# Kernel tuning notes

Hardware: AMD Instinct MI355X
Metric: run time of the kernel (lower is better)

## Reference

```python
import jax, jax.numpy as jnp
import numpy as np

N, E, G = 50000, 500000, 64
F_IN, H, C = 10, 4, 64
HC = H * C  # 256
NCLS = 8
BN_EPS = 1e-5


def _bn(x, g, b, m, v):
    # eval-mode BatchNorm1d with running stats
    return (x - m) * jax.lax.rsqrt(v + BN_EPS) * g + b


def _gat(x, src, dst, W, a_s, a_d, b):
    # PyG GATConv (concat=True): h=[N,H,C]; e_ij=leakyrelu(a_s.h_j + a_d.h_i);
    # softmax over incoming edges of each destination node; scatter-add.
    n = x.shape[0]
    h = (x @ W).reshape(n, H, C)
    es = jnp.einsum('nhc,hc->nh', h, a_s)  # source term per node
    ed = jnp.einsum('nhc,hc->nh', h, a_d)  # dest term per node
    e = jax.nn.leaky_relu(es[src] + ed[dst], 0.2)            # [E2,H]
    m = jax.ops.segment_max(e, dst, num_segments=n)
    ex = jnp.exp(e - m[dst])
    s = jax.ops.segment_sum(ex, dst, num_segments=n)
    alpha = ex / (s[dst] + 1e-16)                             # [E2,H]
    out = jax.ops.segment_sum(h[src] * alpha[:, :, None], dst, num_segments=n)
    return out.reshape(n, HC) + b, alpha


def _gcn(x, src, dst, W, b):
    n = x.shape[0]
    deg = jax.ops.segment_sum(jnp.ones_like(src, dtype=x.dtype), dst, num_segments=n)
    dinv = jax.lax.rsqrt(jnp.maximum(deg, 1.0))
    norm = dinv[src] * dinv[dst]
    xw = x @ W
    return jax.ops.segment_sum(xw[src] * norm[:, None], dst, num_segments=n) + b


def setup_inputs() -> dict:
    key = jax.random.key(0)
    ks = jax.random.split(key, 48)
    r = lambda i, sh, sc=0.1: jax.random.normal(ks[i], sh, dtype=jnp.float32) * sc
    p = {}
    p['x'] = jax.random.normal(ks[0], (N, F_IN), dtype=jnp.float32)
    p['edge_index'] = jax.random.randint(ks[1], (2, E), 0, N, dtype=jnp.int32)
    p['batch'] = jnp.sort(jax.random.randint(ks[2], (N,), 0, G, dtype=jnp.int32))
    # GAT1
    p['W1'] = r(3, (F_IN, HC)); p['as1'] = r(4, (H, C)); p['ad1'] = r(5, (H, C)); p['bi1'] = r(6, (HC,))
    # GAT2
    p['W2'] = r(7, (HC, HC)); p['as2'] = r(8, (H, C)); p['ad2'] = r(9, (H, C)); p['bi2'] = r(10, (HC,))
    # BN running stats / affine
    for i, (nm, d) in enumerate([('bn1', HC), ('bn2', HC), ('bn3', C)]):
        k0 = 11 + 4 * i
        p[nm + '_g'] = 1.0 + r(k0, (d,))
        p[nm + '_b'] = r(k0 + 1, (d,))
        p[nm + '_m'] = r(k0 + 2, (d,))
        p[nm + '_v'] = 1.0 + jax.random.uniform(ks[k0 + 3], (d,), dtype=jnp.float32) * 0.5
    # GCN
    p['Wg'] = r(23, (HC, C)); p['bg'] = r(24, (C,))
    # reduce_dim
    p['Wr'] = r(25, (2 * C, C)); p['br'] = r(26, (C,))
    # rul head
    p['Wh1'] = r(27, (C, 32)); p['bh1'] = r(28, (32,))
    p['Wh2'] = r(29, (32, 16)); p['bh2'] = r(30, (16,))
    p['Wh3'] = r(31, (16, 1)); p['bh3'] = r(32, (1,))
    # location head
    p['Wl1'] = r(33, (C, 32)); p['bl1'] = r(34, (32,))
    p['Wl2'] = r(35, (32, NCLS)); p['bl2'] = r(36, (NCLS,))
    # energy head
    p['We1'] = r(37, (C, 16)); p['be1'] = r(38, (16,))
    p['We2'] = r(39, (16, 1)); p['be2'] = r(40, (1,))
    return p


def reference(x, edge_index, batch,
              W1, as1, ad1, bi1, W2, as2, ad2, bi2,
              bn1_g, bn1_b, bn1_m, bn1_v, bn2_g, bn2_b, bn2_m, bn2_v,
              bn3_g, bn3_b, bn3_m, bn3_v,
              Wg, bg, Wr, br,
              Wh1, bh1, Wh2, bh2, Wh3, bh3,
              Wl1, bl1, Wl2, bl2, We1, be1, We2, be2):
    n = x.shape[0]
    loop = jnp.arange(n, dtype=edge_index.dtype)
    src = jnp.concatenate([edge_index[0], loop])
    dst = jnp.concatenate([edge_index[1], loop])

    h, alpha1 = _gat(x, src, dst, W1, as1, ad1, bi1)
    h = jax.nn.elu(_bn(h, bn1_g, bn1_b, bn1_m, bn1_v))  # dropout = identity (eval)
    h, alpha2 = _gat(h, src, dst, W2, as2, ad2, bi2)
    h = jax.nn.elu(_bn(h, bn2_g, bn2_b, bn2_m, bn2_v))
    h = _gcn(h, src, dst, Wg, bg)
    h = jax.nn.elu(_bn(h, bn3_g, bn3_b, bn3_m, bn3_v))  # node embeddings [N,64]

    cnt = jax.ops.segment_sum(jnp.ones((n,), h.dtype), batch, num_segments=G)
    x_mean = jax.ops.segment_sum(h, batch, num_segments=G) / jnp.maximum(cnt, 1.0)[:, None]
    x_max = jax.ops.segment_max(h, batch, num_segments=G)
    x_max = jnp.where(cnt[:, None] > 0, x_max, 0.0)
    xg = jnp.concatenate([x_mean, x_max], axis=1) @ Wr + br  # [G,64]

    t = jax.nn.relu(xg @ Wh1 + bh1)
    t = jax.nn.relu(t @ Wh2 + bh2)
    rul = jax.nn.sigmoid(t @ Wh3 + bh3) * 100.0
    loc = jax.nn.relu(xg @ Wl1 + bl1) @ Wl2 + bl2
    en = jax.nn.relu(xg @ We1 + be1) @ We2 + be2
    return rul, loc, en, h, xg
```

## Files before the change

kernel.cpp:

```cpp
#include <hip/hip_runtime.h>
#include <math.h>

#define SCAN_BLK 1024
#define BN_EPS 1e-5f

typedef __attribute__((ext_vector_type(8))) short short8;
typedef __attribute__((ext_vector_type(4))) short short4v;
typedef __attribute__((ext_vector_type(4))) float f32x4;

__device__ __forceinline__ float eluf(float x){ return x > 0.f ? x : (expf(x) - 1.f); }
__device__ __forceinline__ unsigned short f2bf(float f){
  unsigned u = __float_as_uint(f);
  u += 0x7FFFu + ((u >> 16) & 1u);
  return (unsigned short)(u >> 16);
}
__device__ __forceinline__ float bf2f(unsigned short s){
  return __uint_as_float(((unsigned)s) << 16);
}
__device__ __forceinline__ unsigned fmap(float f){
  unsigned b = __float_as_uint(f);
  return (b & 0x80000000u) ? ~b : (b | 0x80000000u);
}
__device__ __forceinline__ float funmap(unsigned u){
  unsigned b = (u & 0x80000000u) ? (u ^ 0x80000000u) : ~u;
  return __uint_as_float(b);
}
__device__ __forceinline__ float lrelu(float a){ return a > 0.f ? a : 0.2f * a; }

__global__ void k_count(const int* __restrict__ ei, int* __restrict__ deg, int ne, int e2)
{
  int t = blockIdx.x * 256 + threadIdx.x;
  if (t >= e2) return;
  int dst = (t < ne) ? ei[ne + t] : t - ne;
  atomicAdd(&deg[dst], 1);
}

__global__ void k_scan1(const int* __restrict__ deg, int* __restrict__ rowptr,
                        int* __restrict__ partials, float* __restrict__ dinv, int n)
{
  __shared__ int sh[SCAN_BLK];
  int t = threadIdx.x, base = blockIdx.x * SCAN_BLK;
  int v = (base + t < n) ? deg[base + t] : 0;
  sh[t] = v;
  __syncthreads();
  for (int off = 1; off < SCAN_BLK; off <<= 1) {
    int u = 0;
    if (t >= off) u = sh[t - off];
    __syncthreads();
    if (t >= off) sh[t] += u;
    __syncthreads();
  }
  if (base + t < n) {
    rowptr[base + t] = sh[t] - v;
    dinv[base + t] = rsqrtf(fmaxf((float)v, 1.f));
  }
  if (t == SCAN_BLK - 1) partials[blockIdx.x] = sh[t];
}

__global__ void k_scan2(int* __restrict__ rowptr, const int* __restrict__ partials, int n)
{
  int base = blockIdx.x * SCAN_BLK;
  int add = 0;
  for (int i = 0; i < blockIdx.x; i++) add += partials[i];
  int t = threadIdx.x;
  if (base + t < n) rowptr[base + t] += add;
}

__global__ void k_fill(const int* __restrict__ ei, const int* __restrict__ rowptr,
                       int* __restrict__ cursor, int* __restrict__ col, int ne, int e2)
{
  int t = blockIdx.x * 256 + threadIdx.x;
  if (t >= e2) return;
  int src, dst;
  if (t < ne) { src = ei[t]; dst = ei[ne + t]; } else { src = dst = t - ne; }
  int pos = rowptr[dst] + atomicAdd(&cursor[dst], 1);
  col[pos] = src;
}

__global__ void k_pack(const float* __restrict__ W, unsigned short* __restrict__ Wp,
                       int N, int nct)
{
  int tid = threadIdx.x;
  int l = tid >> 3, j = tid & 7;
  int ct = blockIdx.x >> 3, ks = blockIdx.x & 7;
  int k = ks * 32 + (l >> 4) * 8 + j;
  int c = ct * 16 + (l & 15);
  Wp[(size_t)(ks * nct + ct) * 512 + tid] = f2bf(W[(size_t)k * N + c]);
}

__global__ void k_prep_all(const float* __restrict__ W1, const float* __restrict__ as1,
                           const float* __restrict__ ad1,
                           const float* __restrict__ W2, const float* __restrict__ as2,
                           const float* __restrict__ ad2,
                           const float* __restrict__ bi1, const float* __restrict__ g1,
                           const float* __restrict__ b1, const float* __restrict__ m1,
                           const float* __restrict__ v1,
                           const float* __restrict__ bi2, const float* __restrict__ g2,
                           const float* __restrict__ b2, const float* __restrict__ m2,
                           const float* __restrict__ v2,
                           float* __restrict__ Ws1, float* __restrict__ Wd1,
                           float* __restrict__ WasT,
                           float* __restrict__ A1, float* __restrict__ B1,
                           float* __restrict__ A2, float* __restrict__ B2)
{
  int t = threadIdx.x;
  if (blockIdx.x < 8) {
    int g = blockIdx.x * 256 + t;
    int half = g >= 1024, r = g & 1023;
    int i = r >> 2, h = r & 3;
    const float* a = half ? ad2 : as2;
    float s = 0.f;
    for (int c = 0; c < 64; c++) s += W2[(size_t)i * 256 + h * 64 + c] * a[h * 64 + c];
    WasT[(size_t)(half * 4 + h) * 256 + i] = s;
  } else {
    if (t < 80) {
      int half = t / 40, r = t % 40;
      int k = r / 4, h = r % 4;
      const float* a = half ? ad1 : as1;
      float s = 0.f;
      for (int c = 0; c < 64; c++) s += W1[k * 256 + h * 64 + c] * a[h * 64 + c];
      (half ? Wd1 : Ws1)[k * 4 + h] = s;
    }
    if (t < 256) {
      float a = rsqrtf(v1[t] + BN_EPS) * g1[t];
      A1[t] = a; B1[t] = (bi1[t] - m1[t]) * a + b1[t];
      a = rsqrtf(v2[t] + BN_EPS) * g2[t];
      A2[t] = a; B2[t] = (bi2[t] - m2[t]) * a + b2[t];
    }
  }
}

__global__ void k_es1(const float* __restrict__ x, const float* __restrict__ Ws1,
                      const float* __restrict__ Wd1,
                      float* __restrict__ es, float* __restrict__ ed, int n)
{
  int t = blockIdx.x * 256 + threadIdx.x;
  if (t >= n) return;
  float xr[10];
  #pragma unroll
  for (int k = 0; k < 10; k++) xr[k] = x[(size_t)t * 10 + k];
  float e0[4] = {0,0,0,0}, e1[4] = {0,0,0,0};
  #pragma unroll
  for (int k = 0; k < 10; k++) {
    #pragma unroll
    for (int h = 0; h < 4; h++) {
      e0[h] += xr[k] * Ws1[k * 4 + h];
      e1[h] += xr[k] * Wd1[k * 4 + h];
    }
  }
  *(float4*)&es[t * 4] = make_float4(e0[0], e0[1], e0[2], e0[3]);
  *(float4*)&ed[t * 4] = make_float4(e1[0], e1[1], e1[2], e1[3]);
}

__global__ void k_xagg(const int* __restrict__ rowptr, const int* __restrict__ deg,
                       const int* __restrict__ col,
                       const float* __restrict__ es, const float* __restrict__ ed,
                       const float* __restrict__ x, float* __restrict__ xa, int n)
{
  int d = blockIdx.x * 4 + (threadIdx.x >> 6);
  if (d >= n) return;
  int lane = threadIdx.x & 63;
  int slot = lane >> 4, k = lane & 15;
  int start = rowptr[d], cnt = deg[d];
  bool active = (k < 10);
  float4 edv = *(const float4*)&ed[d * 4];

  float a0 = 0.f, a1 = 0.f, a2 = 0.f, a3 = 0.f;
  float s0 = 0.f, s1 = 0.f, s2 = 0.f, s3 = 0.f;
  int i = slot;
  for (; i + 4 < cnt; i += 8) {
    int e0 = start + i, e1 = start + i + 4;
    int sa = col[e0], sb = col[e1];
    float4 u0 = *(const float4*)&es[sa * 4];
    float4 u1 = *(const float4*)&es[sb * 4];
    float x0 = active ? x[(size_t)sa * 10 + k] : 0.f;
    float x1 = active ? x[(size_t)sb * 10 + k] : 0.f;
    float ex;
    ex = expf(lrelu(u0.x + edv.x)); a0 += ex * x0; s0 += ex;
    ex = expf(lrelu(u0.y + edv.y)); a1 += ex * x0; s1 += ex;
    ex = expf(lrelu(u0.z + edv.z)); a2 += ex * x0; s2 += ex;
    ex = expf(lrelu(u0.w + edv.w)); a3 += ex * x0; s3 += ex;
    ex = expf(lrelu(u1.x + edv.x)); a0 += ex * x1; s0 += ex;
    ex = expf(lrelu(u1.y + edv.y)); a1 += ex * x1; s1 += ex;
    ex = expf(lrelu(u1.z + edv.z)); a2 += ex * x1; s2 += ex;
    ex = expf(lrelu(u1.w + edv.w)); a3 += ex * x1; s3 += ex;
  }
  if (i < cnt) {
    int e0 = start + i;
    int sa = col[e0];
    float4 u0 = *(const float4*)&es[sa * 4];
    float x0 = active ? x[(size_t)sa * 10 + k] : 0.f;
    float ex;
    ex = expf(lrelu(u0.x + edv.x)); a0 += ex * x0; s0 += ex;
    ex = expf(lrelu(u0.y + edv.y)); a1 += ex * x0; s1 += ex;
    ex = expf(lrelu(u0.z + edv.z)); a2 += ex * x0; s2 += ex;
    ex = expf(lrelu(u0.w + edv.w)); a3 += ex * x0; s3 += ex;
  }
  a0 += __shfl_xor(a0, 16, 64); a0 += __shfl_xor(a0, 32, 64);
  a1 += __shfl_xor(a1, 16, 64); a1 += __shfl_xor(a1, 32, 64);
  a2 += __shfl_xor(a2, 16, 64); a2 += __shfl_xor(a2, 32, 64);
  a3 += __shfl_xor(a3, 16, 64); a3 += __shfl_xor(a3, 32, 64);
  s0 += __shfl_xor(s0, 16, 64); s0 += __shfl_xor(s0, 32, 64);
  s1 += __shfl_xor(s1, 16, 64); s1 += __shfl_xor(s1, 32, 64);
  s2 += __shfl_xor(s2, 16, 64); s2 += __shfl_xor(s2, 32, 64);
  s3 += __shfl_xor(s3, 16, 64); s3 += __shfl_xor(s3, 32, 64);

  if (slot == 0 && active) {
    float* xo = &xa[(size_t)d * 40];
    xo[k]      = a0 / (s0 + 1e-16f);
    xo[10 + k] = a1 / (s1 + 1e-16f);
    xo[20 + k] = a2 / (s2 + 1e-16f);
    xo[30 + k] = a3 / (s3 + 1e-16f);
  }
}

__global__ void k_gemm_xa(const float* __restrict__ xa, const float* __restrict__ W1,
                          const float* __restrict__ A1, const float* __restrict__ B1,
                          const float* __restrict__ WasT,
                          unsigned short* __restrict__ actA,
                          float* __restrict__ es, float* __restrict__ ed, int n)
{
  __shared__ float xal[160];
  __shared__ float actl[4][256];
  int tid = threadIdx.x;
  int n0 = blockIdx.x * 4;
  if (tid < 160 && (size_t)n0 * 40 + tid < (size_t)n * 40)
    xal[tid] = xa[(size_t)n0 * 40 + tid];
  __syncthreads();
  int c = tid, h = c >> 6;
  float w[10];
  #pragma unroll
  for (int k = 0; k < 10; k++) w[k] = W1[k * 256 + c];
  float a1 = A1[c], b1 = B1[c];
  #pragma unroll
  for (int m = 0; m < 4; m++) {
    int nn = n0 + m;
    if (nn >= n) break;
    float acc = 0.f;
    #pragma unroll
    for (int k = 0; k < 10; k++) acc += xal[m * 40 + h * 10 + k] * w[k];
    float v = eluf(acc * a1 + b1);
    actl[m][c] = v;
    actA[(size_t)nn * 256 + c] = f2bf(v);
  }
  __syncthreads();
  int wave = tid >> 6, lane = tid & 63;
  int nn = n0 + wave;
  if (nn < n) {
    float e[8] = {0,0,0,0,0,0,0,0};
    int c0 = lane * 4;
    #pragma unroll
    for (int j = 0; j < 4; j++) {
      float av = actl[wave][c0 + j];
      #pragma unroll
      for (int q = 0; q < 8; q++) e[q] += av * WasT[q * 256 + c0 + j];
    }
    #pragma unroll
    for (int off = 1; off < 64; off <<= 1) {
      #pragma unroll
      for (int q = 0; q < 8; q++) e[q] += __shfl_xor(e[q], off, 64);
    }
    if (lane == 0) {
      *(float4*)&es[nn * 4] = make_float4(e[0], e[1], e[2], e[3]);
      *(float4*)&ed[nn * 4] = make_float4(e[4], e[5], e[6], e[7]);
    }
  }
}

__global__ void k_gat_gather(const int* __restrict__ rowptr, const int* __restrict__ deg,
                             const int* __restrict__ col,
                             const float* __restrict__ es, const float* __restrict__ ed,
                             const unsigned short* __restrict__ act,
                             unsigned short* __restrict__ outb, int n)
{
  int d = blockIdx.x * 4 + (threadIdx.x >> 6);
  if (d >= n) return;
  int lane = threadIdx.x & 63;
  int half = lane >> 5, l32 = lane & 31;
  int c8 = l32 * 8, head = l32 >> 3;
  int start = rowptr[d], cnt = deg[d];
  float edh = ed[d * 4 + head];

  float acc[8] = {0.f,0.f,0.f,0.f,0.f,0.f,0.f,0.f};
  float sex = 0.f;
  int T = (cnt > half) ? ((cnt - half + 1) >> 1) : 0;
  int ebase = start + half;
  int t = 0;
  for (; t + 4 <= T; t += 4) {
    int e0 = ebase + 2 * t, e1 = e0 + 2, e2 = e0 + 4, e3 = e0 + 6;
    int s0 = col[e0], s1 = col[e1], s2 = col[e2], s3 = col[e3];
    float x0 = expf(lrelu(es[s0 * 4 + head] + edh));
    float x1 = expf(lrelu(es[s1 * 4 + head] + edh));
    float x2 = expf(lrelu(es[s2 * 4 + head] + edh));
    float x3 = expf(lrelu(es[s3 * 4 + head] + edh));
    short8 h0 = *(const short8*)&act[(size_t)s0 * 256 + c8];
    short8 h1 = *(const short8*)&act[(size_t)s1 * 256 + c8];
    short8 h2 = *(const short8*)&act[(size_t)s2 * 256 + c8];
    short8 h3 = *(const short8*)&act[(size_t)s3 * 256 + c8];
    #pragma unroll
    for (int j = 0; j < 8; j++) {
      acc[j] += bf2f((unsigned short)h0[j]) * x0 + bf2f((unsigned short)h1[j]) * x1
              + bf2f((unsigned short)h2[j]) * x2 + bf2f((unsigned short)h3[j]) * x3;
    }
    sex += x0 + x1 + x2 + x3;
  }
  for (; t < T; t++) {
    int e0 = ebase + 2 * t;
    int s0 = col[e0];
    float x0 = expf(lrelu(es[s0 * 4 + head] + edh));
    short8 h0 = *(const short8*)&act[(size_t)s0 * 256 + c8];
    #pragma unroll
    for (int j = 0; j < 8; j++) acc[j] += bf2f((unsigned short)h0[j]) * x0;
    sex += x0;
  }
  #pragma unroll
  for (int j = 0; j < 8; j++)
    acc[j] += __shfl_xor(acc[j], 32, 64);
  sex += __shfl_xor(sex, 32, 64);

  if (half == 0) {
    float sv = 1.f / (sex + 1e-16f);
    short8 o;
    #pragma unroll
    for (int j = 0; j < 8; j++) o[j] = (short)f2bf(acc[j] * sv);
    *(short8*)&outb[(size_t)d * 256 + c8] = o;
  }
}

__global__ __launch_bounds__(256) void k_mfma_gemm2(
    const unsigned short* __restrict__ agg2, const unsigned short* __restrict__ Wp2,
    const unsigned short* __restrict__ Wpg,
    const float* __restrict__ Abn, const float* __restrict__ Bbn,
    unsigned short* __restrict__ xwb, int n)
{
  __shared__ unsigned short bsh[16 * 512];
  __shared__ unsigned short act2[64 * 264];
  int tid = threadIdx.x, wave = tid >> 6, lane = tid & 63;
  int l15 = lane & 15, lg = lane >> 4;
  int rbase = blockIdx.x * 64 + wave * 16;
  int arow = rbase + l15; if (arow > n - 1) arow = n - 1;
  const unsigned short* ap = &agg2[(size_t)arow * 256 + lg * 8];

  f32x4 acc[16];
  f32x4 z = {0.f, 0.f, 0.f, 0.f};
  #pragma unroll
  for (int ct = 0; ct < 16; ct++) acc[ct] = z;

  for (int ks = 0; ks < 8; ks++) {
    const unsigned short* src = Wp2 + (size_t)ks * 16 * 512 + wave * 16 * 128;
    short8 stg[4];
    #pragma unroll
    for (int c = 0; c < 4; c++)
      stg[c] = *(const short8*)(src + c * 512 + lane * 8);
    short8 a = *(const short8*)(ap + ks * 32);
    __syncthreads();
    #pragma unroll
    for (int c = 0; c < 4; c++)
      *(short8*)&bsh[wave * 16 * 128 + c * 512 + lane * 8] = stg[c];
    __syncthreads();
    #pragma unroll
    for (int ct = 0; ct < 16; ct++) {
      short8 b = *(const short8*)&bsh[(ct * 64 + lane) * 8];
      acc[ct] = __builtin_amdgcn_mfma_f32_16x16x32_bf16(a, b, acc[ct], 0, 0, 0);
    }
  }

  float abn[16], bbn[16];
  #pragma unroll
  for (int ct = 0; ct < 16; ct++) {
    abn[ct] = Abn[ct * 16 + l15];
    bbn[ct] = Bbn[ct * 16 + l15];
  }
  #pragma unroll
  for (int r = 0; r < 4; r++) {
    int row = rbase + lg * 4 + r;
    if (row < n) {
      int rl = wave * 16 + lg * 4 + r;
      #pragma unroll
      for (int ct = 0; ct < 16; ct++) {
        float v = eluf(acc[r < 0 ? 0 : ct][r] * abn[ct] + bbn[ct]);
        act2[rl * 264 + ct * 16 + l15] = f2bf(v);
      }
    }
  }
  __syncthreads();

  f32x4 acc2[4];
  #pragma unroll
  for (int ct = 0; ct < 4; ct++) acc2[ct] = z;
  const unsigned short* a2p = &act2[(wave * 16 + l15) * 264];
  #pragma unroll
  for (int ks = 0; ks < 8; ks++) {
    short8 a2 = *(const short8*)(a2p + ks * 32 + lg * 8);
    #pragma unroll
    for (int ct = 0; ct < 4; ct++) {
      short8 b = *(const short8*)&Wpg[(size_t)(ks * 4 + ct) * 512 + lane * 8];
      acc2[ct] = __builtin_amdgcn_mfma_f32_16x16x32_bf16(a2, b, acc2[ct], 0, 0, 0);
    }
  }
  #pragma unroll
  for (int r = 0; r < 4; r++) {
    int row = rbase + lg * 4 + r;
    if (row < n) {
      #pragma unroll
      for (int ct = 0; ct < 4; ct++)
        xwb[(size_t)row * 64 + ct * 16 + l15] = f2bf(acc2[ct][r]);
    }
  }
}

__global__ void k_gcn_gather(const int* __restrict__ rowptr, const int* __restrict__ deg,
                             const int* __restrict__ col, const float* __restrict__ dinv,
                             const unsigned short* __restrict__ xwb,
                             const float* __restrict__ bias,
                             const float* __restrict__ gg, const float* __restrict__ bb,
                             const float* __restrict__ mm, const float* __restrict__ vv,
                             float* __restrict__ hout, int n)
{
  int d = blockIdx.x * 4 + (threadIdx.x >> 6);
  if (d >= n) return;
  int lane = threadIdx.x & 63;
  int slot = lane >> 3, cg = (lane & 7) * 8;
  int start = rowptr[d], cnt = deg[d];
  float dinvd = rsqrtf(fmaxf((float)cnt, 1.f));

  float acc[8] = {0.f,0.f,0.f,0.f,0.f,0.f,0.f,0.f};
  int i = slot;
  for (; i + 8 < cnt; i += 16) {
    int s0 = col[start + i], s1 = col[start + i + 8];
    float n0 = dinv[s0], n1 = dinv[s1];
    short8 h0 = *(const short8*)&xwb[(size_t)s0 * 64 + cg];
    short8 h1 = *(const short8*)&xwb[(size_t)s1 * 64 + cg];
    #pragma unroll
    for (int j = 0; j < 8; j++)
      acc[j] += bf2f((unsigned short)h0[j]) * n0 + bf2f((unsigned short)h1[j]) * n1;
  }
  if (i < cnt) {
    int s0 = col[start + i];
    float n0 = dinv[s0];
    short8 h0 = *(const short8*)&xwb[(size_t)s0 * 64 + cg];
    #pragma unroll
    for (int j = 0; j < 8; j++)
      acc[j] += bf2f((unsigned short)h0[j]) * n0;
  }
  #pragma unroll
  for (int j = 0; j < 8; j++) {
    acc[j] += __shfl_xor(acc[j], 8, 64);
    acc[j] += __shfl_xor(acc[j], 16, 64);
    acc[j] += __shfl_xor(acc[j], 32, 64);
    acc[j] *= dinvd;
  }

  if (lane < 8) {
    float out[8];
    #pragma unroll
    for (int j = 0; j < 8; j++) {
      int c = cg + j;
      float r = ((acc[j] + bias[c]) - mm[c]) * rsqrtf(vv[c] + BN_EPS) * gg[c] + bb[c];
      out[j] = eluf(r);
    }
    *(float4*)&hout[(size_t)d * 64 + cg]     = make_float4(out[0], out[1], out[2], out[3]);
    *(float4*)&hout[(size_t)d * 64 + cg + 4] = make_float4(out[4], out[5], out[6], out[7]);
  }
}

__global__ void k_pool_partial(const float* __restrict__ hout, const int* __restrict__ batch,
                               float* __restrict__ psum, unsigned* __restrict__ pmaxu,
                               int n)
{
  int wave = threadIdx.x >> 6, lane = threadIdx.x & 63;
  int wbase = blockIdx.x * 128 + wave * 32;
  int wend = wbase + 32; if (wend > n) wend = n;
  if (wbase >= n) return;

  int g_cur = -1;
  float s = 0.f, mx = -1e30f;
  for (int node = wbase; node < wend; node++) {
    int g = batch[node];
    if (g != g_cur) {
      if (g_cur >= 0) {
        atomicAdd(&psum[g_cur * 64 + lane], s);
        atomicMax(&pmaxu[g_cur * 64 + lane], fmap(mx));
      }
      g_cur = g; s = 0.f; mx = -1e30f;
    }
    float v = hout[(size_t)node * 64 + lane];
    s += v;
    mx = fmaxf(mx, v);
  }
  if (g_cur >= 0) {
    atomicAdd(&psum[g_cur * 64 + lane], s);
    atomicMax(&pmaxu[g_cur * 64 + lane], fmap(mx));
  }
}

__global__ void k_heads(const float* __restrict__ psum, const unsigned* __restrict__ pmaxu,
                        const int* __restrict__ batch,
                        const float* __restrict__ Wr, const float* __restrict__ br,
                        const float* __restrict__ Wh1, const float* __restrict__ bh1,
                        const float* __restrict__ Wh2, const float* __restrict__ bh2,
                        const float* __restrict__ Wh3, const float* __restrict__ bh3,
                        const float* __restrict__ Wl1, const float* __restrict__ bl1,
                        const float* __restrict__ Wl2, const float* __restrict__ bl2,
                        const float* __restrict__ We1, const float* __restrict__ be1,
                        const float* __restrict__ We2, const float* __restrict__ be2,
                        float* __restrict__ outp, int n, int xg_off)
{
  __shared__ float cat[128], xg[64], t1[32], t2[16], l1[32], e1[16];
  int g = blockIdx.x, c = threadIdx.x;

  int lo = 0, hi = n;
  while (lo < hi) { int mid = (lo + hi) >> 1; if (batch[mid] < g) lo = mid + 1; else hi = mid; }
  int start = lo;
  lo = start; hi = n;
  while (lo < hi) { int mid = (lo + hi) >> 1; if (batch[mid] < g + 1) lo = mid + 1; else hi = mid; }
  int cntg = lo - start;

  float mean = psum[g * 64 + c] / fmaxf((float)cntg, 1.f);
  float mxv = (cntg > 0) ? funmap(pmaxu[g * 64 + c]) : 0.f;
  cat[c] = mean; cat[64 + c] = mxv;
  __syncthreads();
  float a = br[c];
  for (int i = 0; i < 128; i++) a += cat[i] * Wr[i * 64 + c];
  xg[c] = a;
  outp[xg_off + g * 64 + c] = a;
  __syncthreads();
  if (c < 32) {
    float u = bh1[c]; for (int i = 0; i < 64; i++) u += xg[i] * Wh1[i * 32 + c];
    t1[c] = fmaxf(u, 0.f);
    float v = bl1[c]; for (int i = 0; i < 64; i++) v += xg[i] * Wl1[i * 32 + c];
    l1[c] = fmaxf(v, 0.f);
  }
  __syncthreads();
  if (c < 16) {
    float u = bh2[c]; for (int i = 0; i < 32; i++) u += t1[i] * Wh2[i * 16 + c];
    t2[c] = fmaxf(u, 0.f);
    float v = be1[c]; for (int i = 0; i < 64; i++) v += xg[i] * We1[i * 16 + c];
    e1[c] = fmaxf(v, 0.f);
  }
  __syncthreads();
  if (c < 8) {
    float v = bl2[c]; for (int i = 0; i < 32; i++) v += l1[i] * Wl2[i * 8 + c];
    outp[64 + g * 8 + c] = v;
  }
  if (c == 0) {
    float u = bh3[0]; for (int i = 0; i < 16; i++) u += t2[i] * Wh3[i];
    outp[g] = 100.f / (1.f + expf(-u));
    float v = be2[0]; for (int i = 0; i < 16; i++) v += e1[i] * We2[i];
    outp[576 + g] = v;
  }
}

extern "C" void kernel_launch(void* const* d_in, const int* in_sizes, int n_in,
                              void* d_out, int out_size, void* d_ws, size_t ws_size,
                              hipStream_t stream)
{
  const float* x    = (const float*)d_in[0];
  const int*   ei   = (const int*)d_in[1];
  const int*   batch= (const int*)d_in[2];
  const float* W1   = (const float*)d_in[3];
  const float* as1  = (const float*)d_in[4];
  const float* ad1  = (const float*)d_in[5];
  const float* bi1  = (const float*)d_in[6];
  const float* W2   = (const float*)d_in[7];
  const float* as2  = (const float*)d_in[8];
  const float* ad2  = (const float*)d_in[9];
  const float* bi2  = (const float*)d_in[10];
  const float* bn1g = (const float*)d_in[11];
  const float* bn1b = (const float*)d_in[12];
  const float* bn1m = (const float*)d_in[13];
  const float* bn1v = (const float*)d_in[14];
  const float* bn2g = (const float*)d_in[15];
  const float* bn2b = (const float*)d_in[16];
  const float* bn2m = (const float*)d_in[17];
  const float* bn2v = (const float*)d_in[18];
  const float* bn3g = (const float*)d_in[19];
  const float* bn3b = (const float*)d_in[20];
  const float* bn3m = (const float*)d_in[21];
  const float* bn3v = (const float*)d_in[22];
  const float* Wg   = (const float*)d_in[23];
  const float* bg   = (const float*)d_in[24];
  const float* Wr   = (const float*)d_in[25];
  const float* br   = (const float*)d_in[26];
  const float* Wh1  = (const float*)d_in[27];
  const float* bh1  = (const float*)d_in[28];
  const float* Wh2  = (const float*)d_in[29];
  const float* bh2  = (const float*)d_in[30];
  const float* Wh3  = (const float*)d_in[31];
  const float* bh3  = (const float*)d_in[32];
  const float* Wl1  = (const float*)d_in[33];
  const float* bl1  = (const float*)d_in[34];
  const float* Wl2  = (const float*)d_in[35];
  const float* bl2  = (const float*)d_in[36];
  const float* We1  = (const float*)d_in[37];
  const float* be1  = (const float*)d_in[38];
  const float* We2  = (const float*)d_in[39];
  const float* be2  = (const float*)d_in[40];

  const int n  = in_sizes[2];
  const int ne = in_sizes[1] / 2;
  const int e2 = ne + n;

  float* ws = (float*)d_ws;
  size_t off = 0;
  unsigned short* bufA = (unsigned short*)(ws + off); off += (size_t)n * 128;
  unsigned short* bufB = (unsigned short*)(ws + off); off += (size_t)n * 128;
  float* xa   = ws + off; off += (size_t)n * 40;
  float* es   = ws + off; off += (size_t)n * 4;
  float* ed   = ws + off; off += (size_t)n * 4;
  float* dinv = ws + off; off += (size_t)n;
  int* rowptr = (int*)(ws + off); off += (size_t)n + 1;
  int* deg    = (int*)(ws + off); off += (size_t)n;
  int* cursor = (int*)(ws + off); off += (size_t)n;
  int* col    = (int*)(ws + off); off += (size_t)e2;
  int* partials = (int*)(ws + off); off += 64;
  unsigned short* Wp2 = (unsigned short*)(ws + off); off += 32768;
  unsigned short* Wpg = (unsigned short*)(ws + off); off += 8192;
  float* Ws1  = ws + off; off += 40;
  float* Wd1  = ws + off; off += 40;
  float* WasT = ws + off; off += 2048;
  float* A1   = ws + off; off += 256;
  float* B1   = ws + off; off += 256;
  float* A2   = ws + off; off += 256;
  float* B2   = ws + off; off += 256;
  float* psum = ws + off; off += 64 * 64;
  unsigned* pmaxu = (unsigned*)(ws + off); off += 64 * 64;

  unsigned short* actA = bufA;
  unsigned short* agg2 = bufB;
  unsigned short* xwb  = bufA;

  float* outp = (float*)d_out;
  float* hout = outp + 640;
  const int xg_off = 640 + n * 64;

  const int eb   = (e2 + 255) / 256;
  const int gb1  = (n + 3) / 4;
  const int gmb  = (n + 63) / 64;
  const int nsb  = (n + SCAN_BLK - 1) / SCAN_BLK;

  hipMemsetAsync(deg, 0, (size_t)2 * n * sizeof(int), stream);
  k_count<<<eb, 256, 0, stream>>>(ei, deg, ne, e2);
  k_scan1<<<nsb, SCAN_BLK, 0, stream>>>(deg, rowptr, partials, dinv, n);
  k_scan2<<<nsb, SCAN_BLK, 0, stream>>>(rowptr, partials, n);
  k_fill<<<eb, 256, 0, stream>>>(ei, rowptr, cursor, col, ne, e2);
  k_pack<<<128, 512, 0, stream>>>(W2, Wp2, 256, 16);
  k_pack<<<32, 512, 0, stream>>>(Wg, Wpg, 64, 4);
  k_prep_all<<<9, 256, 0, stream>>>(W1, as1, ad1, W2, as2, ad2,
                                    bi1, bn1g, bn1b, bn1m, bn1v,
                                    bi2, bn2g, bn2b, bn2m, bn2v,
                                    Ws1, Wd1, WasT, A1, B1, A2, B2);

  k_es1<<<(n + 255) / 256, 256, 0, stream>>>(x, Ws1, Wd1, es, ed, n);
  k_xagg<<<gb1, 256, 0, stream>>>(rowptr, deg, col, es, ed, x, xa, n);
  k_gemm_xa<<<gb1, 256, 0, stream>>>(xa, W1, A1, B1, WasT, actA, es, ed, n);

  k_gat_gather<<<gb1, 256, 0, stream>>>(rowptr, deg, col, es, ed, actA, agg2, n);
  k_mfma_gemm2<<<gmb, 256, 0, stream>>>(agg2, Wp2, Wpg, A2, B2, xwb, n);

  k_gcn_gather<<<gb1, 256, 0, stream>>>(rowptr, deg, col, dinv, xwb,
                                        bg, bn3g, bn3b, bn3m, bn3v, hout, n);

  hipMemsetAsync(psum, 0, 2 * 64 * 64 * sizeof(float), stream);
  k_pool_partial<<<(n + 127) / 128, 256, 0, stream>>>(hout, batch, psum, pmaxu, n);
  k_heads<<<64, 64, 0, stream>>>(psum, pmaxu, batch, Wr, br,
                                 Wh1, bh1, Wh2, bh2, Wh3, bh3,
                                 Wl1, bl1, Wl2, bl2, We1, be1, We2, be2,
                                 outp, n, xg_off);
}
```

Baseline: 288.0 us.

## Fuse setup kernels and give each GAT destination node a half-wave

Merges the two weight-pack launches and the prep launch into one kernel, and merges degree counting with the first-layer attention-score computation, which cuts the number of small kernel launches. The GAT gather now assigns one destination node to a 32-lane half-wave instead of splitting its edges across two halves of a 64-lane wave. This removes the cross-half shuffle reduction and doubles the number of nodes per block. The trade-off is a longer serial edge loop per node. It also drops a dead ternary in the gemm2 epilogue.

```diff
diff --git a/kernel.cpp b/kernel.cpp
--- a/kernel.cpp
+++ b/kernel.cpp
@@ -27,12 +27,94 @@
 }
 __device__ __forceinline__ float lrelu(float a){ return a > 0.f ? a : 0.2f * a; }
 
-__global__ void k_count(const int* __restrict__ ei, int* __restrict__ deg, int ne, int e2)
-{
-  int t = blockIdx.x * 256 + threadIdx.x;
-  if (t >= e2) return;
-  int dst = (t < ne) ? ei[ne + t] : t - ne;
-  atomicAdd(&deg[dst], 1);
+__global__ void k_pack_prep(const float* __restrict__ W1, const float* __restrict__ as1,
+                            const float* __restrict__ ad1,
+                            const float* __restrict__ W2, const float* __restrict__ as2,
+                            const float* __restrict__ ad2,
+                            const float* __restrict__ Wg,
+                            const float* __restrict__ bi1, const float* __restrict__ g1,
+                            const float* __restrict__ b1, const float* __restrict__ m1,
+                            const float* __restrict__ v1,
+                            const float* __restrict__ bi2, const float* __restrict__ g2,
+                            const float* __restrict__ b2, const float* __restrict__ m2,
+                            const float* __restrict__ v2,
+                            unsigned short* __restrict__ Wp2, unsigned short* __restrict__ Wpg,
+                            float* __restrict__ Ws1, float* __restrict__ Wd1,
+                            float* __restrict__ WasT,
+                            float* __restrict__ A1, float* __restrict__ B1,
+                            float* __restrict__ A2, float* __restrict__ B2)
+{
+  int b = blockIdx.x, tid = threadIdx.x;
+  if (b < 128) {
+    int l = tid >> 3, j = tid & 7;
+    int ct = b >> 3, ks = b & 7;
+    int k = ks * 32 + (l >> 4) * 8 + j;
+    int c = ct * 16 + (l & 15);
+    Wp2[(size_t)(ks * 16 + ct) * 512 + tid] = f2bf(W2[(size_t)k * 256 + c]);
+  } else if (b < 160) {
+    int bb = b - 128;
+    int l = tid >> 3, j = tid & 7;
+    int ct = bb >> 3, ks = bb & 7;
+    int k = ks * 32 + (l >> 4) * 8 + j;
+    int c = ct * 16 + (l & 15);
+    Wpg[(size_t)(ks * 4 + ct) * 512 + tid] = f2bf(Wg[(size_t)k * 64 + c]);
+  } else if (b < 168) {
+    if (tid < 256) {
+      int g = (b - 160) * 256 + tid;
+      int half = g >= 1024, r = g & 1023;
+      int i = r >> 2, h = r & 3;
+      const float* a = half ? ad2 : as2;
+      float s = 0.f;
+      for (int c = 0; c < 64; c++) s += W2[(size_t)i * 256 + h * 64 + c] * a[h * 64 + c];
+      WasT[(size_t)(half * 4 + h) * 256 + i] = s;
+    }
+  } else {
+    if (tid < 80) {
+      int half = tid / 40, r = tid % 40;
+      int k = r / 4, h = r % 4;
+      const float* a = half ? ad1 : as1;
+      float s = 0.f;
+      for (int c = 0; c < 64; c++) s += W1[k * 256 + h * 64 + c] * a[h * 64 + c];
+      (half ? Wd1 : Ws1)[k * 4 + h] = s;
+    }
+    if (tid < 256) {
+      float a = rsqrtf(v1[tid] + BN_EPS) * g1[tid];
+      A1[tid] = a; B1[tid] = (bi1[tid] - m1[tid]) * a + b1[tid];
+      a = rsqrtf(v2[tid] + BN_EPS) * g2[tid];
+      A2[tid] = a; B2[tid] = (bi2[tid] - m2[tid]) * a + b2[tid];
+    }
+  }
+}
+
+__global__ void k_count_es1(const int* __restrict__ ei, int* __restrict__ deg,
+                            const float* __restrict__ x,
+                            const float* __restrict__ Ws1, const float* __restrict__ Wd1,
+                            float* __restrict__ es, float* __restrict__ ed,
+                            int ne, int e2, int n, int eb)
+{
+  if (blockIdx.x < eb) {
+    int t = blockIdx.x * 256 + threadIdx.x;
+    if (t >= e2) return;
+    int dst = (t < ne) ? ei[ne + t] : t - ne;
+    atomicAdd(&deg[dst], 1);
+  } else {
+    int t = (blockIdx.x - eb) * 256 + threadIdx.x;
+    if (t >= n) return;
+    float xr[10];
+    #pragma unroll
+    for (int k = 0; k < 10; k++) xr[k] = x[(size_t)t * 10 + k];
+    float e0[4] = {0,0,0,0}, e1[4] = {0,0,0,0};
+    #pragma unroll
+    for (int k = 0; k < 10; k++) {
+      #pragma unroll
+      for (int h = 0; h < 4; h++) {
+        e0[h] += xr[k] * Ws1[k * 4 + h];
+        e1[h] += xr[k] * Wd1[k * 4 + h];
+      }
+    }
+    *(float4*)&es[t * 4] = make_float4(e0[0], e0[1], e0[2], e0[3]);
+    *(float4*)&ed[t * 4] = make_float4(e1[0], e1[1], e1[2], e1[3]);
+  }
 }
 
 __global__ void k_scan1(const int* __restrict__ deg, int* __restrict__ rowptr,
@@ -75,81 +157,6 @@
   if (t < ne) { src = ei[t]; dst = ei[ne + t]; } else { src = dst = t - ne; }
   int pos = rowptr[dst] + atomicAdd(&cursor[dst], 1);
   col[pos] = src;
-}
-
-__global__ void k_pack(const float* __restrict__ W, unsigned short* __restrict__ Wp,
-                       int N, int nct)
-{
-  int tid = threadIdx.x;
-  int l = tid >> 3, j = tid & 7;
-  int ct = blockIdx.x >> 3, ks = blockIdx.x & 7;
-  int k = ks * 32 + (l >> 4) * 8 + j;
-  int c = ct * 16 + (l & 15);
-  Wp[(size_t)(ks * nct + ct) * 512 + tid] = f2bf(W[(size_t)k * N + c]);
-}
-
-__global__ void k_prep_all(const float* __restrict__ W1, const float* __restrict__ as1,
-                           const float* __restrict__ ad1,
-                           const float* __restrict__ W2, const float* __restrict__ as2,
-                           const float* __restrict__ ad2,
-                           const float* __restrict__ bi1, const float* __restrict__ g1,
-                           const float* __restrict__ b1, const float* __restrict__ m1,
-                           const float* __restrict__ v1,
-                           const float* __restrict__ bi2, const float* __restrict__ g2,
-                           const float* __restrict__ b2, const float* __restrict__ m2,
-                           const float* __restrict__ v2,
-                           float* __restrict__ Ws1, float* __restrict__ Wd1,
-                           float* __restrict__ WasT,
-                           float* __restrict__ A1, float* __restrict__ B1,
-                           float* __restrict__ A2, float* __restrict__ B2)
-{
-  int t = threadIdx.x;
-  if (blockIdx.x < 8) {
-    int g = blockIdx.x * 256 + t;
-    int half = g >= 1024, r = g & 1023;
-    int i = r >> 2, h = r & 3;
-    const float* a = half ? ad2 : as2;
-    float s = 0.f;
-    for (int c = 0; c < 64; c++) s += W2[(size_t)i * 256 + h * 64 + c] * a[h * 64 + c];
-    WasT[(size_t)(half * 4 + h) * 256 + i] = s;
-  } else {
-    if (t < 80) {
-      int half = t / 40, r = t % 40;
-      int k = r / 4, h = r % 4;
-      const float* a = half ? ad1 : as1;
-      float s = 0.f;
-      for (int c = 0; c < 64; c++) s += W1[k * 256 + h * 64 + c] * a[h * 64 + c];
-      (half ? Wd1 : Ws1)[k * 4 + h] = s;
-    }
-    if (t < 256) {
-      float a = rsqrtf(v1[t] + BN_EPS) * g1[t];
-      A1[t] = a; B1[t] = (bi1[t] - m1[t]) * a + b1[t];
-      a = rsqrtf(v2[t] + BN_EPS) * g2[t];
-      A2[t] = a; B2[t] = (bi2[t] - m2[t]) * a + b2[t];
-    }
-  }
-}
-
-__global__ void k_es1(const float* __restrict__ x, const float* __restrict__ Ws1,
-                      const float* __restrict__ Wd1,
-                      float* __restrict__ es, float* __restrict__ ed, int n)
-{
-  int t = blockIdx.x * 256 + threadIdx.x;
-  if (t >= n) return;
-  float xr[10];
-  #pragma unroll
-  for (int k = 0; k < 10; k++) xr[k] = x[(size_t)t * 10 + k];
-  float e0[4] = {0,0,0,0}, e1[4] = {0,0,0,0};
-  #pragma unroll
-  for (int k = 0; k < 10; k++) {
-    #pragma unroll
-    for (int h = 0; h < 4; h++) {
-      e0[h] += xr[k] * Ws1[k * 4 + h];
-      e1[h] += xr[k] * Wd1[k * 4 + h];
-    }
-  }
-  *(float4*)&es[t * 4] = make_float4(e0[0], e0[1], e0[2], e0[3]);
-  *(float4*)&ed[t * 4] = make_float4(e1[0], e1[1], e1[2], e1[3]);
 }
 
 __global__ void k_xagg(const int* __restrict__ rowptr, const int* __restrict__ deg,
@@ -273,22 +280,20 @@
                              const unsigned short* __restrict__ act,
                              unsigned short* __restrict__ outb, int n)
 {
-  int d = blockIdx.x * 4 + (threadIdx.x >> 6);
+  int hw = threadIdx.x >> 5;
+  int d = blockIdx.x * 8 + hw;
   if (d >= n) return;
-  int lane = threadIdx.x & 63;
-  int half = lane >> 5, l32 = lane & 31;
+  int l32 = threadIdx.x & 31;
   int c8 = l32 * 8, head = l32 >> 3;
   int start = rowptr[d], cnt = deg[d];
   float edh = ed[d * 4 + head];
 
   float acc[8] = {0.f,0.f,0.f,0.f,0.f,0.f,0.f,0.f};
   float sex = 0.f;
-  int T = (cnt > half) ? ((cnt - half + 1) >> 1) : 0;
-  int ebase = start + half;
-  int t = 0;
-  for (; t + 4 <= T; t += 4) {
-    int e0 = ebase + 2 * t, e1 = e0 + 2, e2 = e0 + 4, e3 = e0 + 6;
-    int s0 = col[e0], s1 = col[e1], s2 = col[e2], s3 = col[e3];
+  int i = 0;
+  for (; i + 4 <= cnt; i += 4) {
+    int e0 = start + i;
+    int s0 = col[e0], s1 = col[e0 + 1], s2 = col[e0 + 2], s3 = col[e0 + 3];
     float x0 = expf(lrelu(es[s0 * 4 + head] + edh));
     float x1 = expf(lrelu(es[s1 * 4 + head] + edh));
     float x2 = expf(lrelu(es[s2 * 4 + head] + edh));
@@ -304,8 +309,8 @@
     }
     sex += x0 + x1 + x2 + x3;
   }
-  for (; t < T; t++) {
-    int e0 = ebase + 2 * t;
+  for (; i < cnt; i++) {
+    int e0 = start + i;
     int s0 = col[e0];
     float x0 = expf(lrelu(es[s0 * 4 + head] + edh));
     short8 h0 = *(const short8*)&act[(size_t)s0 * 256 + c8];
@@ -313,18 +318,11 @@
     for (int j = 0; j < 8; j++) acc[j] += bf2f((unsigned short)h0[j]) * x0;
     sex += x0;
   }
-  #pragma unroll
-  for (int j = 0; j < 8; j++)
-    acc[j] += __shfl_xor(acc[j], 32, 64);
-  sex += __shfl_xor(sex, 32, 64);
-
-  if (half == 0) {
-    float sv = 1.f / (sex + 1e-16f);
-    short8 o;
-    #pragma unroll
-    for (int j = 0; j < 8; j++) o[j] = (short)f2bf(acc[j] * sv);
-    *(short8*)&outb[(size_t)d * 256 + c8] = o;
-  }
+  float sv = 1.f / (sex + 1e-16f);
+  short8 o;
+  #pragma unroll
+  for (int j = 0; j < 8; j++) o[j] = (short)f2bf(acc[j] * sv);
+  *(short8*)&outb[(size_t)d * 256 + c8] = o;
 }
 
 __global__ __launch_bounds__(256) void k_mfma_gemm2(
@@ -378,7 +376,7 @@
       int rl = wave * 16 + lg * 4 + r;
       #pragma unroll
       for (int ct = 0; ct < 16; ct++) {
-        float v = eluf(acc[r < 0 ? 0 : ct][r] * abn[ct] + bbn[ct]);
+        float v = eluf(acc[ct][r] * abn[ct] + bbn[ct]);
         act2[rl * 264 + ct * 16 + l15] = f2bf(v);
       }
     }
@@ -635,27 +633,26 @@
   const int xg_off = 640 + n * 64;
 
   const int eb   = (e2 + 255) / 256;
+  const int nb1  = (n + 255) / 256;
   const int gb1  = (n + 3) / 4;
+  const int gb8  = (n + 7) / 8;
   const int gmb  = (n + 63) / 64;
   const int nsb  = (n + SCAN_BLK - 1) / SCAN_BLK;
 
   hipMemsetAsync(deg, 0, (size_t)2 * n * sizeof(int), stream);
-  k_count<<<eb, 256, 0, stream>>>(ei, deg, ne, e2);
+  k_pack_prep<<<169, 512, 0, stream>>>(W1, as1, ad1, W2, as2, ad2, Wg,
+                                       bi1, bn1g, bn1b, bn1m, bn1v,
+                                       bi2, bn2g, bn2b, bn2m, bn2v,
+                                       Wp2, Wpg, Ws1, Wd1, WasT, A1, B1, A2, B2);
+  k_count_es1<<<eb + nb1, 256, 0, stream>>>(ei, deg, x, Ws1, Wd1, es, ed, ne, e2, n, eb);
   k_scan1<<<nsb, SCAN_BLK, 0, stream>>>(deg, rowptr, partials, dinv, n);
   k_scan2<<<nsb, SCAN_BLK, 0, stream>>>(rowptr, partials, n);
   k_fill<<<eb, 256, 0, stream>>>(ei, rowptr, cursor, col, ne, e2);
-  k_pack<<<128, 512, 0, stream>>>(W2, Wp2, 256, 16);
-  k_pack<<<32, 512, 0, stream>>>(Wg, Wpg, 64, 4);
-  k_prep_all<<<9, 256, 0, stream>>>(W1, as1, ad1, W2, as2, ad2,
-                                    bi1, bn1g, bn1b, bn1m, bn1v,
-                                    bi2, bn2g, bn2b, bn2m, bn2v,
-                                    Ws1, Wd1, WasT, A1, B1, A2, B2);
-
-  k_es1<<<(n + 255) / 256, 256, 0, stream>>>(x, Ws1, Wd1, es, ed, n);
+
   k_xagg<<<gb1, 256, 0, stream>>>(rowptr, deg, col, es, ed, x, xa, n);
   k_gemm_xa<<<gb1, 256, 0, stream>>>(xa, W1, A1, B1, WasT, actA, es, ed, n);
 
-  k_gat_gather<<<gb1, 256, 0, stream>>>(rowptr, deg, col, es, ed, actA, agg2, n);
+  k_gat_gather<<<gb8, 256, 0, stream>>>(rowptr, deg, col, es, ed, actA, agg2, n);
   k_mfma_gemm2<<<gmb, 256, 0, stream>>>(agg2, Wp2, Wpg, A2, B2, xwb, n);
 
   k_gcn_gather<<<gb1, 256, 0, stream>>>(rowptr, deg, col, dinv, xwb,
```

Result: faster. 282.3 us (-2.0%).
